# Performance work log

Measured on AMD Instinct MI355X. Metric: run time of the kernel, lower is better.

The kernel has to match this reference:

```python
import jax, jax.numpy as jnp
import numpy as np

B, L, D, H = 4, 512, 256, 128  # batch, seq_len, input_size, hidden_size
NEG = -1e30


def setup_inputs() -> dict:
    key = jax.random.key(0)
    ks = jax.random.split(key, 16)
    init = lambda k, shape, fan_in: (jax.random.normal(k, shape, jnp.float32) / np.sqrt(fan_in).astype(np.float32))
    v = jax.random.normal(ks[0], (B, L, D), jnp.float32)
    lengths = jax.random.randint(ks[1], (B,), L // 2, L + 1).astype(jnp.int32)
    p_mask = (jnp.arange(L)[None, :] < lengths[:, None])  # [B, L] bool
    return {
        "v": v,
        "lengths": lengths,
        "p_mask": p_mask,
        "own_W": init(ks[2], (H, D), D), "own_b": jnp.zeros((H,), jnp.float32),
        "comp_W": init(ks[3], (H, D), D), "comp_b": jnp.zeros((H,), jnp.float32),
        "v_attn": init(ks[4], (H,), H),
        "gate_W": init(ks[5], (2 * D, 2 * D), 2 * D), "gate_b": jnp.zeros((2 * D,), jnp.float32),
        "w_ih_f": init(ks[6], (3 * H, 2 * D), 2 * D), "w_hh_f": init(ks[7], (3 * H, H), H),
        "b_ih_f": jnp.zeros((3 * H,), jnp.float32), "b_hh_f": jnp.zeros((3 * H,), jnp.float32),
        "w_ih_b": init(ks[8], (3 * H, 2 * D), 2 * D), "w_hh_b": init(ks[9], (3 * H, H), H),
        "b_ih_b": jnp.zeros((3 * H,), jnp.float32), "b_hh_b": jnp.zeros((3 * H,), jnp.float32),
    }


def _gru(x, tmask, w_ih, w_hh, b_ih, b_hh, reverse):
    """Single-direction GRU over [B, L, In] with length masking (emulates packing)."""
    Bn, Ln, _ = x.shape
    Hn = w_hh.shape[1]
    xp = jnp.einsum('bli,hi->blh', x, w_ih) + b_ih  # [B, L, 3H] input projections

    def step(h, inputs):
        xpt, m = inputs  # [B, 3H], [B, 1]
        hp = h @ w_hh.T + b_hh
        xr, xz, xn = jnp.split(xpt, 3, axis=-1)
        hr, hz, hn = jnp.split(hp, 3, axis=-1)
        r = jax.nn.sigmoid(xr + hr)
        z = jax.nn.sigmoid(xz + hz)
        n = jnp.tanh(xn + r * hn)
        h_new = (1.0 - z) * n + z * h
        h = jnp.where(m, h_new, h)
        return h, jnp.where(m, h_new, jnp.zeros_like(h_new))

    h0 = jnp.zeros((Bn, Hn), x.dtype)
    xs = (jnp.swapaxes(xp, 0, 1), tmask.T[:, :, None])
    _, outs = jax.lax.scan(step, h0, xs, reverse=reverse)
    return jnp.swapaxes(outs, 0, 1)  # [B, L, H]


def reference(v, lengths, p_mask, own_W, own_b, comp_W, comp_b, v_attn,
              gate_W, gate_b, w_ih_f, w_hh_f, b_ih_f, b_hh_f,
              w_ih_b, w_hh_b, b_ih_b, b_hh_b):
    # Additive (Bahdanau / RNet) self-attention, vectorized over all query positions.
    own = v @ own_W.T + own_b    # [B, L, H] (query term)
    comp = v @ comp_W.T + comp_b  # [B, L, H] (key term)
    # scores[b, q, k] = tanh(own_q + comp_k) . v_attn
    scores = jnp.einsum('bqkh,h->bqk', jnp.tanh(own[:, :, None, :] + comp[:, None, :, :]), v_attn)
    scores = jnp.where(p_mask[:, None, :], scores, NEG)  # mask padded keys
    attn = jax.nn.softmax(scores, axis=2)
    C = jnp.einsum('bqk,bkd->bqd', attn, v)  # attended context
    inp = jnp.concatenate([v, C], axis=-1)   # [B, L, 2D]
    inp = jax.nn.sigmoid(inp @ gate_W.T + gate_b) * inp  # gating
    # Bidirectional GRU encoder (pack_padded emulated via time mask; eval mode, no dropout).
    tmask = (jnp.arange(inp.shape[1])[None, :] < lengths[:, None])
    out_f = _gru(inp, tmask, w_ih_f, w_hh_f, b_ih_f, b_hh_f, reverse=False)
    out_b = _gru(inp, tmask, w_ih_b, w_hh_b, b_ih_b, b_hh_b, reverse=True)
    return jnp.concatenate([out_f, out_b], axis=-1)  # [B, L, 2H]
```

## Files before the change

### kernel.cpp

```cpp
#include <hip/hip_runtime.h>
#include <hip/hip_bf16.h>

#define NEGINF -1e30f

typedef __attribute__((ext_vector_type(8))) short short8;
typedef __attribute__((ext_vector_type(4))) float f32x4;

__device__ __forceinline__ float fast_sigmoid(float x) {
    return __builtin_amdgcn_rcpf(1.f + __expf(-x));
}
__device__ __forceinline__ float fast_tanh(float x) {
    return 1.f - 2.f * __builtin_amdgcn_rcpf(1.f + __expf(2.f * x));
}
__device__ __forceinline__ short f2bf(float f) {
    unsigned u = __float_as_uint(f);
    return (short)((u + 0x7fff + ((u >> 16) & 1)) >> 16);
}
__device__ __forceinline__ float bf2f(short b) {
    return __uint_as_float(((unsigned)(unsigned short)b) << 16);
}

__device__ __forceinline__ void bar_lds() {
    asm volatile("s_waitcnt lgkmcnt(0)\n\ts_barrier" ::: "memory");
}

__global__ __launch_bounds__(256) void gemm_bias(
    const float* __restrict__ A,
    const float* __restrict__ W1, const float* __restrict__ b1, float* __restrict__ out1,
    const float* __restrict__ W2, const float* __restrict__ b2, float* __restrict__ out2,
    const int* __restrict__ lengths,
    int M, int N, int K, int nsplit, int mode) {
    const int m0 = blockIdx.y * 64;
    if ((m0 & 511) >= lengths[m0 >> 9]) return;
    __shared__ __align__(16) short Abh[2][2048];
    __shared__ __align__(16) short Abl[2][2048];
    __shared__ __align__(16) short Bbh[2][2048];
    __shared__ __align__(16) short Bbl[2][2048];
    const int tid = threadIdx.x;
    int bx = blockIdx.x;
    const float* W = W1; const float* bias = b1; float* out = out1;
    int n0;
    if (bx < nsplit) {
        n0 = bx * 64;
    } else {
        W = W2; bias = b2; out = out2;
        n0 = (bx - nsplit) * 64;
    }
    const int wave = tid >> 6;
    const int lane = tid & 63;
    const int mrow = lane & 15;
    const int quad = lane >> 4;
    const int wm = (wave >> 1) * 32;
    const int wn = (wave & 1) * 32;

    const int r_ = tid >> 2;
    const int sg = (tid & 3) * 8;

    f32x4 acc[2][2];
#pragma unroll
    for (int mt = 0; mt < 2; mt++)
#pragma unroll
        for (int nt = 0; nt < 2; nt++) acc[mt][nt] = (f32x4){0.f, 0.f, 0.f, 0.f};

    float4 a0 = *(const float4*)(A + (size_t)(m0 + r_) * K + sg);
    float4 a1 = *(const float4*)(A + (size_t)(m0 + r_) * K + sg + 4);
    float4 w0 = *(const float4*)(W + (size_t)(n0 + r_) * K + sg);
    float4 w1 = *(const float4*)(W + (size_t)(n0 + r_) * K + sg + 4);

    for (int k0 = 0; k0 < K; k0 += 32) {
        const int cur = (k0 >> 5) & 1;
        {
            float av[8] = {a0.x, a0.y, a0.z, a0.w, a1.x, a1.y, a1.z, a1.w};
            float wv[8] = {w0.x, w0.y, w0.z, w0.w, w1.x, w1.y, w1.z, w1.w};
            short8 ah, al, bh, bl;
#pragma unroll
            for (int j = 0; j < 8; j++) {
                short h = f2bf(av[j]); ah[j] = h; al[j] = f2bf(av[j] - bf2f(h));
                short g = f2bf(wv[j]); bh[j] = g; bl[j] = f2bf(wv[j] - bf2f(g));
            }
            *(short8*)&Abh[cur][r_ * 32 + sg] = ah;
            *(short8*)&Abl[cur][r_ * 32 + sg] = al;
            *(short8*)&Bbh[cur][r_ * 32 + sg] = bh;
            *(short8*)&Bbl[cur][r_ * 32 + sg] = bl;
        }
        if (k0 + 32 < K) {
            a0 = *(const float4*)(A + (size_t)(m0 + r_) * K + k0 + 32 + sg);
            a1 = *(const float4*)(A + (size_t)(m0 + r_) * K + k0 + 32 + sg + 4);
            w0 = *(const float4*)(W + (size_t)(n0 + r_) * K + k0 + 32 + sg);
            w1 = *(const float4*)(W + (size_t)(n0 + r_) * K + k0 + 32 + sg + 4);
        }
        bar_lds();
        short8 Ah[2], Al[2], Bh[2], Bl[2];
#pragma unroll
        for (int t = 0; t < 2; t++) {
            int ar = (wm + t * 16 + mrow) * 32 + quad * 8;
            int br = (wn + t * 16 + mrow) * 32 + quad * 8;
            Ah[t] = *(const short8*)&Abh[cur][ar];
            Al[t] = *(const short8*)&Abl[cur][ar];
            Bh[t] = *(const short8*)&Bbh[cur][br];
            Bl[t] = *(const short8*)&Bbl[cur][br];
        }
#pragma unroll
        for (int mt = 0; mt < 2; mt++)
#pragma unroll
            for (int nt = 0; nt < 2; nt++) {
                acc[mt][nt] = __builtin_amdgcn_mfma_f32_16x16x32_bf16(Ah[mt], Bh[nt], acc[mt][nt], 0, 0, 0);
                acc[mt][nt] = __builtin_amdgcn_mfma_f32_16x16x32_bf16(Al[mt], Bh[nt], acc[mt][nt], 0, 0, 0);
                acc[mt][nt] = __builtin_amdgcn_mfma_f32_16x16x32_bf16(Ah[mt], Bl[nt], acc[mt][nt], 0, 0, 0);
            }
        bar_lds();
    }
    float bsv[2];
#pragma unroll
    for (int nt = 0; nt < 2; nt++) bsv[nt] = bias[n0 + wn + nt * 16 + mrow];
#pragma unroll
    for (int mt = 0; mt < 2; mt++)
#pragma unroll
        for (int nt = 0; nt < 2; nt++) {
            int n = n0 + wn + nt * 16 + mrow;
#pragma unroll
            for (int r = 0; r < 4; r++) {
                int m = m0 + wm + mt * 16 + quad * 4 + r;
                float val = acc[mt][nt][r] + bsv[nt];
                if (mode == 1) val = fast_sigmoid(val) * A[(size_t)m * K + n];
                out[(size_t)m * N + n] = val;
            }
        }
}

__global__ __launch_bounds__(512) void attn_kernel(
    const float* __restrict__ v, const int* __restrict__ lengths,
    const float* __restrict__ own, const float* __restrict__ comp,
    const float* __restrict__ v_attn, float* __restrict__ inp) {
    const int L = 512, D = 256, H = 128;
    const int b = blockIdx.x >> 6;
    const int q0 = (blockIdx.x & 63) * 8;
    const int len = lengths[b];
    if (q0 >= len) return;
    const int tid = threadIdx.x;
    const float K2E = 2.8853900817779268f;
    __shared__ __align__(16) float oKT[128 * 8];
    __shared__ float va2s[128];
    __shared__ __align__(16) float scf[512 * 12];
    __shared__ float inv8[8];

    for (int i = tid; i < 1024; i += 512) {
        int qq = i >> 7, hh = i & 127;
        oKT[hh * 8 + qq] = K2E * own[((size_t)(b * L + q0 + qq)) * H + hh];
    }
    if (tid < 128) va2s[tid] = -2.f * v_attn[tid];
    __syncthreads();

    {
        const int k = tid;
        float acc[8];
#pragma unroll
        for (int q = 0; q < 8; q++) acc[q] = 0.f;
        if (k < len) {
            const float* cp = comp + ((size_t)(b * L + k)) * H;
            for (int h = 0; h < 128; h += 4) {
                float4 c4 = *(const float4*)(cp + h);
                const float* cv = (const float*)&c4;
#pragma unroll
                for (int j = 0; j < 4; j++) {
                    float cK = cv[j] * K2E;
                    float va = va2s[h + j];
                    float4 o0 = *(const float4*)&oKT[(h + j) * 8];
                    float4 o1 = *(const float4*)&oKT[(h + j) * 8 + 4];
                    const float* op0 = (const float*)&o0;
                    const float* op1 = (const float*)&o1;
#pragma unroll
                    for (int q = 0; q < 4; q++) {
                        float r = __builtin_amdgcn_rcpf(1.f + exp2f(cK + op0[q]));
                        acc[q] = fmaf(va, r, acc[q]);
                    }
#pragma unroll
                    for (int q = 0; q < 4; q++) {
                        float r = __builtin_amdgcn_rcpf(1.f + exp2f(cK + op1[q]));
                        acc[4 + q] = fmaf(va, r, acc[4 + q]);
                    }
                }
            }
#pragma unroll
            for (int q = 0; q < 8; q++) acc[q] = __expf(acc[q]);
        }
        *(float4*)&scf[k * 12] = *(float4*)&acc[0];
        *(float4*)&scf[k * 12 + 4] = *(float4*)&acc[4];
    }
    __syncthreads();

    {
        int w = tid >> 6, l = tid & 63;
        float s = 0.f;
#pragma unroll
        for (int kk = 0; kk < 8; kk++) s += scf[(l + kk * 64) * 12 + w];
#pragma unroll
        for (int off = 1; off < 64; off <<= 1) s += __shfl_xor(s, off);
        if (l == 0) inv8[w] = __builtin_amdgcn_rcpf(s);
    }
    __syncthreads();

    {
        const int d = tid & 255;
        const int qh = tid >> 8;
        float c0 = 0.f, c1 = 0.f, c2 = 0.f, c3 = 0.f;
        const float* vb = v + ((size_t)b * L) * D + d;
        for (int k = 0; k < L; k += 2) {
            float v0 = vb[(size_t)k * D];
            float v1 = vb[(size_t)(k + 1) * D];
            float4 s0 = *(const float4*)&scf[k * 12 + qh * 4];
            float4 s1 = *(const float4*)&scf[(k + 1) * 12 + qh * 4];
            c0 += s0.x * v0 + s1.x * v1;
            c1 += s0.y * v0 + s1.y * v1;
            c2 += s0.z * v0 + s1.z * v1;
            c3 += s0.w * v0 + s1.w * v1;
        }
        float cc[4] = {c0, c1, c2, c3};
#pragma unroll
        for (int j = 0; j < 4; j++) {
            int q = q0 + qh * 4 + j;
            size_t row = ((size_t)(b * L + q)) * 512;
            inp[row + 256 + d] = cc[j] * inv8[qh * 4 + j];
            inp[row + d] = v[((size_t)(b * L + q)) * D + d];
        }
    }
}

__global__ __launch_bounds__(512, 2) void gru_kernel(
    const float* __restrict__ xp_f, const float* __restrict__ xp_b,
    const float* __restrict__ w_hh_f, const float* __restrict__ w_hh_b,
    const float* __restrict__ b_hh_f, const float* __restrict__ b_hh_b,
    const int* __restrict__ lengths, float* __restrict__ out) {
    const int L = 512, H = 128;
    const int dir = blockIdx.x >> 2;
    const int b = blockIdx.x & 3;
    const float* xp = dir ? xp_b : xp_f;
    const float* w_hh = dir ? w_hh_b : w_hh_f;
    const float* b_hh = dir ? b_hh_b : b_hh_f;
    const int tid = threadIdx.x;
    const int wave = tid >> 6;
    const int lane = tid & 63;
    const int mrow = lane & 15;
    const int quad = lane >> 4;
    const int jj = 16 * wave + lane;

    __shared__ __align__(16) short hbuf[2][256];
    __shared__ __align__(16) float xbuf[16 * 384];
    __shared__ __align__(16) float obuf[16 * 128];

    short8 wb[3][4];
#pragma unroll
    for (int g = 0; g < 3; g++) {
        int row = g * 128 + 16 * wave + mrow;
#pragma unroll
        for (int kt = 0; kt < 4; kt++) {
            const float* wp = w_hh + (size_t)row * H + kt * 32 + quad * 8;
            float4 w0 = *(const float4*)(wp);
            float4 w1 = *(const float4*)(wp + 4);
            float wv[8] = {w0.x, w0.y, w0.z, w0.w, w1.x, w1.y, w1.z, w1.w};
            short8 hi8;
#pragma unroll
            for (int k = 0; k < 8; k++) hi8[k] = f2bf(wv[k]);
            wb[g][kt] = hi8;
        }
    }
    float br = 0.f, bz = 0.f, bn = 0.f, hcur = 0.f;
    if (lane < 16) {
        br = b_hh[jj];
        bz = b_hh[128 + jj];
        bn = b_hh[256 + jj];
    }

    const int len = lengths[b];
    for (int idx = tid; idx < (L - len) * 128; idx += 512) {
        int tt = len + (idx >> 7);
        int kk = idx & 127;
        out[((size_t)(b * L + tt)) * 256 + dir * 128 + kk] = 0.f;
    }
    if (tid < 256) hbuf[0][tid] = 0;

    const int f1 = tid + 512, f2 = tid + 1024;
    const int sA = tid / 96, jA = (tid % 96) * 4;
    const int sB = f1 / 96, jB = (f1 % 96) * 4;
    const int sC = f2 / 96, jC = (f2 % 96) * 4;

    const int nch = (len + 15) >> 4;
    float4 r0, r1, r2;
    {
        int tA = dir ? (len - 1 - sA) : sA;
        int tB = dir ? (len - 1 - sB) : sB;
        int tC = dir ? (len - 1 - sC) : sC;
        r0 = *(const float4*)&xp[((size_t)(b * L + tA)) * 384 + jA];
        r1 = *(const float4*)&xp[((size_t)(b * L + tB)) * 384 + jB];
        r2 = *(const float4*)&xp[((size_t)(b * L + tC)) * 384 + jC];
    }
    __syncthreads();

    const int bbase = (mrow & 1) * 128 + quad * 8;
    int par = 0;

    for (int c = 0; c < nch; c++) {
        const int cnt = min(16, len - c * 16);
        if (sA < cnt) *(float4*)&xbuf[sA * 384 + jA] = r0;
        if (sB < cnt) *(float4*)&xbuf[sB * 384 + jB] = r1;
        if (sC < cnt) *(float4*)&xbuf[sC * 384 + jC] = r2;
        if (c > 0) {
            int p0 = (c - 1) * 16;
            for (int i = tid; i < 16 * 128; i += 512) {
                int ss = i >> 7, kk = i & 127;
                int tt = dir ? (len - 1 - (p0 + ss)) : (p0 + ss);
                out[((size_t)(b * L + tt)) * 256 + dir * 128 + kk] = obuf[i];
            }
        }
        if (c + 1 < nch) {
            int ncnt = min(16, len - (c + 1) * 16);
            int base = (c + 1) * 16;
            if (sA < ncnt) {
                int tt = dir ? (len - 1 - (base + sA)) : (base + sA);
                r0 = *(const float4*)&xp[((size_t)(b * L + tt)) * 384 + jA];
            }
            if (sB < ncnt) {
                int tt = dir ? (len - 1 - (base + sB)) : (base + sB);
                r1 = *(const float4*)&xp[((size_t)(b * L + tt)) * 384 + jB];
            }
            if (sC < ncnt) {
                int tt = dir ? (len - 1 - (base + sC)) : (base + sC);
                r2 = *(const float4*)&xp[((size_t)(b * L + tt)) * 384 + jC];
            }
        }
        bar_lds();
        for (int s = 0; s < cnt; s++) {
            float xr, xz, xn;
            if (lane < 16) {
                xr = xbuf[s * 384 + jj];
                xz = xbuf[s * 384 + 128 + jj];
                xn = xbuf[s * 384 + 256 + jj];
            }
            short8 af[4];
#pragma unroll
            for (int kt = 0; kt < 4; kt++) af[kt] = *(const short8*)&hbuf[par][bbase + kt * 32];
            f32x4 acc[3];
#pragma unroll
            for (int g = 0; g < 3; g++) acc[g] = (f32x4){0.f, 0.f, 0.f, 0.f};
#pragma unroll
            for (int kt = 0; kt < 4; kt++)
#pragma unroll
                for (int g = 0; g < 3; g++)
                    acc[g] = __builtin_amdgcn_mfma_f32_16x16x32_bf16(af[kt], wb[g][kt], acc[g], 0, 0, 0);
            if (lane < 16) {
                float hr = acc[0][0] + acc[0][1] + br;
                float hz = acc[1][0] + acc[1][1] + bz;
                float hh = acc[2][0] + acc[2][1] + bn;
                float r = fast_sigmoid(xr + hr);
                float z = fast_sigmoid(xz + hz);
                float n = fast_tanh(xn + r * hh);
                float hn = (1.f - z) * n + z * hcur;
                hcur = hn;
                short hb = f2bf(hn);
                hbuf[par ^ 1][jj] = hb;
                hbuf[par ^ 1][128 + jj] = f2bf(hn - bf2f(hb));
                obuf[s * 128 + jj] = hn;
            }
            par ^= 1;
            bar_lds();
        }
    }
    {
        int p0 = (nch - 1) * 16;
        int pcnt = len - p0;
        for (int i = tid; i < pcnt * 128; i += 512) {
            int ss = i >> 7, kk = i & 127;
            int tt = dir ? (len - 1 - (p0 + ss)) : (p0 + ss);
            out[((size_t)(b * L + tt)) * 256 + dir * 128 + kk] = obuf[i];
        }
    }
}

extern "C" void kernel_launch(void* const* d_in, const int* in_sizes, int n_in,
                              void* d_out, int out_size, void* d_ws, size_t ws_size,
                              hipStream_t stream) {
    const int B = 4, L = 512, D = 256, H = 128;
    const int M = B * L;

    const float* v      = (const float*)d_in[0];
    const int* lengths  = (const int*)d_in[1];
    const float* own_W  = (const float*)d_in[3];
    const float* own_b  = (const float*)d_in[4];
    const float* comp_W = (const float*)d_in[5];
    const float* comp_b = (const float*)d_in[6];
    const float* v_attn = (const float*)d_in[7];
    const float* gate_W = (const float*)d_in[8];
    const float* gate_b = (const float*)d_in[9];
    const float* w_ih_f = (const float*)d_in[10];
    const float* w_hh_f = (const float*)d_in[11];
    const float* b_ih_f = (const float*)d_in[12];
    const float* b_hh_f = (const float*)d_in[13];
    const float* w_ih_b = (const float*)d_in[14];
    const float* w_hh_b = (const float*)d_in[15];
    const float* b_ih_b = (const float*)d_in[16];
    const float* b_hh_b = (const float*)d_in[17];

    float* ws   = (float*)d_ws;
    float* own  = ws;
    float* comp = own + (size_t)M * H;
    float* inp  = comp + (size_t)M * H;
    float* gated = inp + (size_t)M * 512;
    float* xp_f = gated + (size_t)M * 512;
    float* xp_b = xp_f + (size_t)M * 384;
    float* out  = (float*)d_out;

    gemm_bias<<<dim3(4, M / 64), 256, 0, stream>>>(
        v, own_W, own_b, own, comp_W, comp_b, comp, lengths, M, H, D, 2, 0);
    attn_kernel<<<dim3(B * 64), 512, 0, stream>>>(v, lengths, own, comp, v_attn, inp);
    gemm_bias<<<dim3(8, M / 64), 256, 0, stream>>>(
        inp, gate_W, gate_b, gated, gate_W, gate_b, gated, lengths, M, 512, 512, 8, 1);
    gemm_bias<<<dim3(12, M / 64), 256, 0, stream>>>(
        gated, w_ih_f, b_ih_f, xp_f, w_ih_b, b_ih_b, xp_b, lengths, M, 384, 512, 6, 0);
    gru_kernel<<<dim3(8), 512, 0, stream>>>(xp_f, xp_b, w_hh_f, w_hh_b, b_hh_f, b_hh_b, lengths, out);
}
```

Measured before the change: 399.6 us.

## Fuse all stages into one cooperative persistent kernel with grid syncs

Replaces the five separate launches with a single cooperative kernel of 256 blocks of 512 threads. It runs the projection GEMMs, attention, gating GEMM, input-projection GEMM and the GRU recurrence as phases separated by grid.sync, with a shared-memory union across phases. The GEMM tile is reworked for 8 waves, each computing a 32x16 sub-tile with 4-wide loads, and the trailing barrier of each K-step is dropped. The goal is to remove per-launch overhead and inter-kernel gaps. In exchange it pays grid-wide barrier costs, forces occupancy to one block per CU, and leaves most blocks idle during the long GRU phase.

```diff
diff --git a/kernel.cpp b/kernel.cpp
--- a/kernel.cpp
+++ b/kernel.cpp
@@ -1,9 +1,11 @@
 #include <hip/hip_runtime.h>
 #include <hip/hip_bf16.h>
-
-#define NEGINF -1e30f
+#include <hip/hip_cooperative_groups.h>
+
+namespace cg = cooperative_groups;
 
 typedef __attribute__((ext_vector_type(8))) short short8;
+typedef __attribute__((ext_vector_type(4))) short short4_t;
 typedef __attribute__((ext_vector_type(4))) float f32x4;
 
 __device__ __forceinline__ float fast_sigmoid(float x) {
@@ -19,136 +21,107 @@
 __device__ __forceinline__ float bf2f(short b) {
     return __uint_as_float(((unsigned)(unsigned short)b) << 16);
 }
-
 __device__ __forceinline__ void bar_lds() {
     asm volatile("s_waitcnt lgkmcnt(0)\n\ts_barrier" ::: "memory");
 }
 
-__global__ __launch_bounds__(256) void gemm_bias(
-    const float* __restrict__ A,
-    const float* __restrict__ W1, const float* __restrict__ b1, float* __restrict__ out1,
-    const float* __restrict__ W2, const float* __restrict__ b2, float* __restrict__ out2,
-    const int* __restrict__ lengths,
-    int M, int N, int K, int nsplit, int mode) {
-    const int m0 = blockIdx.y * 64;
-    if ((m0 & 511) >= lengths[m0 >> 9]) return;
-    __shared__ __align__(16) short Abh[2][2048];
-    __shared__ __align__(16) short Abl[2][2048];
-    __shared__ __align__(16) short Bbh[2][2048];
-    __shared__ __align__(16) short Bbl[2][2048];
+struct __align__(16) GemmSh { short Abh[2][2048]; short Abl[2][2048];
+                              short Bbh[2][2048]; short Bbl[2][2048]; };
+struct __align__(16) AttnSh { float oKT[1024]; float va2s[128]; float inv8[8];
+                              float scf[6144]; };
+struct __align__(16) GruSh  { short hbuf[2][256]; float xbuf[6144];
+                              float obuf[2048]; };
+union __align__(16) SharedMem { GemmSh g; AttnSh a; GruSh r; };
+
+__device__ void gemm_tile(GemmSh& sh,
+                          const float* __restrict__ A, const float* __restrict__ W,
+                          const float* __restrict__ bias, float* __restrict__ out,
+                          int m0, int n0, int N, int K, int mode) {
     const int tid = threadIdx.x;
-    int bx = blockIdx.x;
-    const float* W = W1; const float* bias = b1; float* out = out1;
-    int n0;
-    if (bx < nsplit) {
-        n0 = bx * 64;
-    } else {
-        W = W2; bias = b2; out = out2;
-        n0 = (bx - nsplit) * 64;
-    }
-    const int wave = tid >> 6;
-    const int lane = tid & 63;
-    const int mrow = lane & 15;
-    const int quad = lane >> 4;
-    const int wm = (wave >> 1) * 32;
-    const int wn = (wave & 1) * 32;
-
-    const int r_ = tid >> 2;
-    const int sg = (tid & 3) * 8;
-
-    f32x4 acc[2][2];
-#pragma unroll
-    for (int mt = 0; mt < 2; mt++)
-#pragma unroll
-        for (int nt = 0; nt < 2; nt++) acc[mt][nt] = (f32x4){0.f, 0.f, 0.f, 0.f};
-
-    float4 a0 = *(const float4*)(A + (size_t)(m0 + r_) * K + sg);
-    float4 a1 = *(const float4*)(A + (size_t)(m0 + r_) * K + sg + 4);
-    float4 w0 = *(const float4*)(W + (size_t)(n0 + r_) * K + sg);
-    float4 w1 = *(const float4*)(W + (size_t)(n0 + r_) * K + sg + 4);
+    const int wave = tid >> 6, lane = tid & 63;
+    const int mrow = lane & 15, quad = lane >> 4;
+    const int wm = (wave >> 2) * 32, wn = (wave & 3) * 16;
+    const int r_ = tid >> 3;
+    const int sg = (tid & 7) * 4;
+
+    bar_lds();
+
+    f32x4 acc[2];
+    acc[0] = (f32x4){0.f, 0.f, 0.f, 0.f};
+    acc[1] = (f32x4){0.f, 0.f, 0.f, 0.f};
+
+    float4 a = *(const float4*)(A + (size_t)(m0 + r_) * K + sg);
+    float4 w = *(const float4*)(W + (size_t)(n0 + r_) * K + sg);
 
     for (int k0 = 0; k0 < K; k0 += 32) {
         const int cur = (k0 >> 5) & 1;
         {
-            float av[8] = {a0.x, a0.y, a0.z, a0.w, a1.x, a1.y, a1.z, a1.w};
-            float wv[8] = {w0.x, w0.y, w0.z, w0.w, w1.x, w1.y, w1.z, w1.w};
-            short8 ah, al, bh, bl;
-#pragma unroll
-            for (int j = 0; j < 8; j++) {
+            float av[4] = {a.x, a.y, a.z, a.w};
+            float wv[4] = {w.x, w.y, w.z, w.w};
+            short4_t ah, al, bh, bl;
+#pragma unroll
+            for (int j = 0; j < 4; j++) {
                 short h = f2bf(av[j]); ah[j] = h; al[j] = f2bf(av[j] - bf2f(h));
                 short g = f2bf(wv[j]); bh[j] = g; bl[j] = f2bf(wv[j] - bf2f(g));
             }
-            *(short8*)&Abh[cur][r_ * 32 + sg] = ah;
-            *(short8*)&Abl[cur][r_ * 32 + sg] = al;
-            *(short8*)&Bbh[cur][r_ * 32 + sg] = bh;
-            *(short8*)&Bbl[cur][r_ * 32 + sg] = bl;
+            *(short4_t*)&sh.Abh[cur][r_ * 32 + sg] = ah;
+            *(short4_t*)&sh.Abl[cur][r_ * 32 + sg] = al;
+            *(short4_t*)&sh.Bbh[cur][r_ * 32 + sg] = bh;
+            *(short4_t*)&sh.Bbl[cur][r_ * 32 + sg] = bl;
         }
         if (k0 + 32 < K) {
-            a0 = *(const float4*)(A + (size_t)(m0 + r_) * K + k0 + 32 + sg);
-            a1 = *(const float4*)(A + (size_t)(m0 + r_) * K + k0 + 32 + sg + 4);
-            w0 = *(const float4*)(W + (size_t)(n0 + r_) * K + k0 + 32 + sg);
-            w1 = *(const float4*)(W + (size_t)(n0 + r_) * K + k0 + 32 + sg + 4);
+            a = *(const float4*)(A + (size_t)(m0 + r_) * K + k0 + 32 + sg);
+            w = *(const float4*)(W + (size_t)(n0 + r_) * K + k0 + 32 + sg);
         }
         bar_lds();
-        short8 Ah[2], Al[2], Bh[2], Bl[2];
-#pragma unroll
-        for (int t = 0; t < 2; t++) {
-            int ar = (wm + t * 16 + mrow) * 32 + quad * 8;
-            int br = (wn + t * 16 + mrow) * 32 + quad * 8;
-            Ah[t] = *(const short8*)&Abh[cur][ar];
-            Al[t] = *(const short8*)&Abl[cur][ar];
-            Bh[t] = *(const short8*)&Bbh[cur][br];
-            Bl[t] = *(const short8*)&Bbl[cur][br];
-        }
-#pragma unroll
-        for (int mt = 0; mt < 2; mt++)
-#pragma unroll
-            for (int nt = 0; nt < 2; nt++) {
-                acc[mt][nt] = __builtin_amdgcn_mfma_f32_16x16x32_bf16(Ah[mt], Bh[nt], acc[mt][nt], 0, 0, 0);
-                acc[mt][nt] = __builtin_amdgcn_mfma_f32_16x16x32_bf16(Al[mt], Bh[nt], acc[mt][nt], 0, 0, 0);
-                acc[mt][nt] = __builtin_amdgcn_mfma_f32_16x16x32_bf16(Ah[mt], Bl[nt], acc[mt][nt], 0, 0, 0);
-            }
-        bar_lds();
-    }
-    float bsv[2];
-#pragma unroll
-    for (int nt = 0; nt < 2; nt++) bsv[nt] = bias[n0 + wn + nt * 16 + mrow];
+        short8 Ah[2], Al[2];
+#pragma unroll
+        for (int mt = 0; mt < 2; mt++) {
+            int ar = (wm + mt * 16 + mrow) * 32 + quad * 8;
+            Ah[mt] = *(const short8*)&sh.Abh[cur][ar];
+            Al[mt] = *(const short8*)&sh.Abl[cur][ar];
+        }
+        int br = (wn + mrow) * 32 + quad * 8;
+        short8 Bh = *(const short8*)&sh.Bbh[cur][br];
+        short8 Bl = *(const short8*)&sh.Bbl[cur][br];
+#pragma unroll
+        for (int mt = 0; mt < 2; mt++) {
+            acc[mt] = __builtin_amdgcn_mfma_f32_16x16x32_bf16(Ah[mt], Bh, acc[mt], 0, 0, 0);
+            acc[mt] = __builtin_amdgcn_mfma_f32_16x16x32_bf16(Al[mt], Bh, acc[mt], 0, 0, 0);
+            acc[mt] = __builtin_amdgcn_mfma_f32_16x16x32_bf16(Ah[mt], Bl, acc[mt], 0, 0, 0);
+        }
+    }
+    const int n = n0 + wn + mrow;
+    const float bsv = bias[n];
 #pragma unroll
     for (int mt = 0; mt < 2; mt++)
 #pragma unroll
-        for (int nt = 0; nt < 2; nt++) {
-            int n = n0 + wn + nt * 16 + mrow;
-#pragma unroll
-            for (int r = 0; r < 4; r++) {
-                int m = m0 + wm + mt * 16 + quad * 4 + r;
-                float val = acc[mt][nt][r] + bsv[nt];
-                if (mode == 1) val = fast_sigmoid(val) * A[(size_t)m * K + n];
-                out[(size_t)m * N + n] = val;
-            }
-        }
-}
-
-__global__ __launch_bounds__(512) void attn_kernel(
-    const float* __restrict__ v, const int* __restrict__ lengths,
-    const float* __restrict__ own, const float* __restrict__ comp,
-    const float* __restrict__ v_attn, float* __restrict__ inp) {
+        for (int r = 0; r < 4; r++) {
+            int m = m0 + wm + mt * 16 + quad * 4 + r;
+            float val = acc[mt][r] + bsv;
+            if (mode == 1) val = fast_sigmoid(val) * A[(size_t)m * K + n];
+            out[(size_t)m * N + n] = val;
+        }
+}
+
+__device__ void attn_block(AttnSh& sh, const float* __restrict__ v,
+                           const int* __restrict__ lengths,
+                           const float* __restrict__ own, const float* __restrict__ comp,
+                           const float* __restrict__ v_attn, float* __restrict__ inp,
+                           int job) {
     const int L = 512, D = 256, H = 128;
-    const int b = blockIdx.x >> 6;
-    const int q0 = (blockIdx.x & 63) * 8;
+    const int b = job >> 6;
+    const int q0 = (job & 63) * 8;
     const int len = lengths[b];
     if (q0 >= len) return;
     const int tid = threadIdx.x;
     const float K2E = 2.8853900817779268f;
-    __shared__ __align__(16) float oKT[128 * 8];
-    __shared__ float va2s[128];
-    __shared__ __align__(16) float scf[512 * 12];
-    __shared__ float inv8[8];
 
     for (int i = tid; i < 1024; i += 512) {
         int qq = i >> 7, hh = i & 127;
-        oKT[hh * 8 + qq] = K2E * own[((size_t)(b * L + q0 + qq)) * H + hh];
-    }
-    if (tid < 128) va2s[tid] = -2.f * v_attn[tid];
+        sh.oKT[hh * 8 + qq] = K2E * own[((size_t)(b * L + q0 + qq)) * H + hh];
+    }
+    if (tid < 128) sh.va2s[tid] = -2.f * v_attn[tid];
     __syncthreads();
 
     {
@@ -164,9 +137,9 @@
 #pragma unroll
                 for (int j = 0; j < 4; j++) {
                     float cK = cv[j] * K2E;
-                    float va = va2s[h + j];
-                    float4 o0 = *(const float4*)&oKT[(h + j) * 8];
-                    float4 o1 = *(const float4*)&oKT[(h + j) * 8 + 4];
+                    float va = sh.va2s[h + j];
+                    float4 o0 = *(const float4*)&sh.oKT[(h + j) * 8];
+                    float4 o1 = *(const float4*)&sh.oKT[(h + j) * 8 + 4];
                     const float* op0 = (const float*)&o0;
                     const float* op1 = (const float*)&o1;
 #pragma unroll
@@ -184,8 +157,8 @@
 #pragma unroll
             for (int q = 0; q < 8; q++) acc[q] = __expf(acc[q]);
         }
-        *(float4*)&scf[k * 12] = *(float4*)&acc[0];
-        *(float4*)&scf[k * 12 + 4] = *(float4*)&acc[4];
+        *(float4*)&sh.scf[k * 12] = *(float4*)&acc[0];
+        *(float4*)&sh.scf[k * 12 + 4] = *(float4*)&acc[4];
     }
     __syncthreads();
 
@@ -193,10 +166,10 @@
         int w = tid >> 6, l = tid & 63;
         float s = 0.f;
 #pragma unroll
-        for (int kk = 0; kk < 8; kk++) s += scf[(l + kk * 64) * 12 + w];
+        for (int kk = 0; kk < 8; kk++) s += sh.scf[(l + kk * 64) * 12 + w];
 #pragma unroll
         for (int off = 1; off < 64; off <<= 1) s += __shfl_xor(s, off);
-        if (l == 0) inv8[w] = __builtin_amdgcn_rcpf(s);
+        if (l == 0) sh.inv8[w] = __builtin_amdgcn_rcpf(s);
     }
     __syncthreads();
 
@@ -208,8 +181,8 @@
         for (int k = 0; k < L; k += 2) {
             float v0 = vb[(size_t)k * D];
             float v1 = vb[(size_t)(k + 1) * D];
-            float4 s0 = *(const float4*)&scf[k * 12 + qh * 4];
-            float4 s1 = *(const float4*)&scf[(k + 1) * 12 + qh * 4];
+            float4 s0 = *(const float4*)&sh.scf[k * 12 + qh * 4];
+            float4 s1 = *(const float4*)&sh.scf[(k + 1) * 12 + qh * 4];
             c0 += s0.x * v0 + s1.x * v1;
             c1 += s0.y * v0 + s1.y * v1;
             c2 += s0.z * v0 + s1.z * v1;
@@ -220,20 +193,20 @@
         for (int j = 0; j < 4; j++) {
             int q = q0 + qh * 4 + j;
             size_t row = ((size_t)(b * L + q)) * 512;
-            inp[row + 256 + d] = cc[j] * inv8[qh * 4 + j];
+            inp[row + 256 + d] = cc[j] * sh.inv8[qh * 4 + j];
             inp[row + d] = v[((size_t)(b * L + q)) * D + d];
         }
     }
 }
 
-__global__ __launch_bounds__(512, 2) void gru_kernel(
-    const float* __restrict__ xp_f, const float* __restrict__ xp_b,
-    const float* __restrict__ w_hh_f, const float* __restrict__ w_hh_b,
-    const float* __restrict__ b_hh_f, const float* __restrict__ b_hh_b,
-    const int* __restrict__ lengths, float* __restrict__ out) {
+__device__ void gru_seq(GruSh& sh,
+                        const float* __restrict__ xp_f, const float* __restrict__ xp_b,
+                        const float* __restrict__ w_hh_f, const float* __restrict__ w_hh_b,
+                        const float* __restrict__ b_hh_f, const float* __restrict__ b_hh_b,
+                        const int* __restrict__ lengths, float* __restrict__ out, int idx) {
     const int L = 512, H = 128;
-    const int dir = blockIdx.x >> 2;
-    const int b = blockIdx.x & 3;
+    const int dir = idx >> 2;
+    const int b = idx & 3;
     const float* xp = dir ? xp_b : xp_f;
     const float* w_hh = dir ? w_hh_b : w_hh_f;
     const float* b_hh = dir ? b_hh_b : b_hh_f;
@@ -244,10 +217,6 @@
     const int quad = lane >> 4;
     const int jj = 16 * wave + lane;
 
-    __shared__ __align__(16) short hbuf[2][256];
-    __shared__ __align__(16) float xbuf[16 * 384];
-    __shared__ __align__(16) float obuf[16 * 128];
-
     short8 wb[3][4];
 #pragma unroll
     for (int g = 0; g < 3; g++) {
@@ -272,12 +241,12 @@
     }
 
     const int len = lengths[b];
-    for (int idx = tid; idx < (L - len) * 128; idx += 512) {
-        int tt = len + (idx >> 7);
-        int kk = idx & 127;
+    for (int i = tid; i < (L - len) * 128; i += 512) {
+        int tt = len + (i >> 7);
+        int kk = i & 127;
         out[((size_t)(b * L + tt)) * 256 + dir * 128 + kk] = 0.f;
     }
-    if (tid < 256) hbuf[0][tid] = 0;
+    if (tid < 256) sh.hbuf[0][tid] = 0;
 
     const int f1 = tid + 512, f2 = tid + 1024;
     const int sA = tid / 96, jA = (tid % 96) * 4;
@@ -301,15 +270,15 @@
 
     for (int c = 0; c < nch; c++) {
         const int cnt = min(16, len - c * 16);
-        if (sA < cnt) *(float4*)&xbuf[sA * 384 + jA] = r0;
-        if (sB < cnt) *(float4*)&xbuf[sB * 384 + jB] = r1;
-        if (sC < cnt) *(float4*)&xbuf[sC * 384 + jC] = r2;
+        if (sA < cnt) *(float4*)&sh.xbuf[sA * 384 + jA] = r0;
+        if (sB < cnt) *(float4*)&sh.xbuf[sB * 384 + jB] = r1;
+        if (sC < cnt) *(float4*)&sh.xbuf[sC * 384 + jC] = r2;
         if (c > 0) {
             int p0 = (c - 1) * 16;
             for (int i = tid; i < 16 * 128; i += 512) {
                 int ss = i >> 7, kk = i & 127;
                 int tt = dir ? (len - 1 - (p0 + ss)) : (p0 + ss);
-                out[((size_t)(b * L + tt)) * 256 + dir * 128 + kk] = obuf[i];
+                out[((size_t)(b * L + tt)) * 256 + dir * 128 + kk] = sh.obuf[i];
             }
         }
         if (c + 1 < nch) {
@@ -332,13 +301,13 @@
         for (int s = 0; s < cnt; s++) {
             float xr, xz, xn;
             if (lane < 16) {
-                xr = xbuf[s * 384 + jj];
-                xz = xbuf[s * 384 + 128 + jj];
-                xn = xbuf[s * 384 + 256 + jj];
+                xr = sh.xbuf[s * 384 + jj];
+                xz = sh.xbuf[s * 384 + 128 + jj];
+                xn = sh.xbuf[s * 384 + 256 + jj];
             }
             short8 af[4];
 #pragma unroll
-            for (int kt = 0; kt < 4; kt++) af[kt] = *(const short8*)&hbuf[par][bbase + kt * 32];
+            for (int kt = 0; kt < 4; kt++) af[kt] = *(const short8*)&sh.hbuf[par][bbase + kt * 32];
             f32x4 acc[3];
 #pragma unroll
             for (int g = 0; g < 3; g++) acc[g] = (f32x4){0.f, 0.f, 0.f, 0.f};
@@ -357,9 +326,9 @@
                 float hn = (1.f - z) * n + z * hcur;
                 hcur = hn;
                 short hb = f2bf(hn);
-                hbuf[par ^ 1][jj] = hb;
-                hbuf[par ^ 1][128 + jj] = f2bf(hn - bf2f(hb));
-                obuf[s * 128 + jj] = hn;
+                sh.hbuf[par ^ 1][jj] = hb;
+                sh.hbuf[par ^ 1][128 + jj] = f2bf(hn - bf2f(hb));
+                sh.obuf[s * 128 + jj] = hn;
             }
             par ^= 1;
             bar_lds();
@@ -371,16 +340,61 @@
         for (int i = tid; i < pcnt * 128; i += 512) {
             int ss = i >> 7, kk = i & 127;
             int tt = dir ? (len - 1 - (p0 + ss)) : (p0 + ss);
-            out[((size_t)(b * L + tt)) * 256 + dir * 128 + kk] = obuf[i];
-        }
-    }
+            out[((size_t)(b * L + tt)) * 256 + dir * 128 + kk] = sh.obuf[i];
+        }
+    }
+}
+
+__global__ __launch_bounds__(512, 1) void mega_kernel(
+    const float* v, const int* lengths,
+    const float* own_W, const float* own_b,
+    const float* comp_W, const float* comp_b,
+    const float* v_attn,
+    const float* gate_W, const float* gate_b,
+    const float* w_ih_f, const float* b_ih_f,
+    const float* w_hh_f, const float* b_hh_f,
+    const float* w_ih_b, const float* b_ih_b,
+    const float* w_hh_b, const float* b_hh_b,
+    float* own, float* comp, float* inp, float* gated,
+    float* xp_f, float* xp_b, float* out) {
+    __shared__ SharedMem sh;
+    cg::grid_group grid = cg::this_grid();
+    const int blk = blockIdx.x;
+
+    if (blk < 128) {
+        int bx = blk & 3, by = blk >> 2;
+        int m0 = by * 64;
+        if ((m0 & 511) < lengths[m0 >> 9]) {
+            if (bx < 2) gemm_tile(sh.g, v, own_W, own_b, own, m0, bx * 64, 128, 256, 0);
+            else        gemm_tile(sh.g, v, comp_W, comp_b, comp, m0, (bx - 2) * 64, 128, 256, 0);
+        }
+    }
+    grid.sync();
+    attn_block(sh.a, v, lengths, own, comp, v_attn, inp, blk);
+    grid.sync();
+    {
+        int bx = blk & 7, by = blk >> 3;
+        int m0 = by * 64;
+        if ((m0 & 511) < lengths[m0 >> 9])
+            gemm_tile(sh.g, inp, gate_W, gate_b, gated, m0, bx * 64, 512, 512, 1);
+    }
+    grid.sync();
+    for (int j = blk; j < 384; j += 256) {
+        int bx = j % 12, by = j / 12;
+        int m0 = by * 64;
+        if ((m0 & 511) >= lengths[m0 >> 9]) continue;
+        if (bx < 6) gemm_tile(sh.g, gated, w_ih_f, b_ih_f, xp_f, m0, bx * 64, 384, 512, 0);
+        else        gemm_tile(sh.g, gated, w_ih_b, b_ih_b, xp_b, m0, (bx - 6) * 64, 384, 512, 0);
+    }
+    grid.sync();
+    if (blk < 8)
+        gru_seq(sh.r, xp_f, xp_b, w_hh_f, w_hh_b, b_hh_f, b_hh_b, lengths, out, blk);
 }
 
 extern "C" void kernel_launch(void* const* d_in, const int* in_sizes, int n_in,
                               void* d_out, int out_size, void* d_ws, size_t ws_size,
                               hipStream_t stream) {
-    const int B = 4, L = 512, D = 256, H = 128;
-    const int M = B * L;
+    const int M = 2048, H = 128;
 
     const float* v      = (const float*)d_in[0];
     const int* lengths  = (const int*)d_in[1];
@@ -400,21 +414,25 @@
     const float* b_ih_b = (const float*)d_in[16];
     const float* b_hh_b = (const float*)d_in[17];
 
-    float* ws   = (float*)d_ws;
-    float* own  = ws;
-    float* comp = own + (size_t)M * H;
-    float* inp  = comp + (size_t)M * H;
+    float* ws    = (float*)d_ws;
+    float* own   = ws;
+    float* comp  = own + (size_t)M * H;
+    float* inp   = comp + (size_t)M * H;
     float* gated = inp + (size_t)M * 512;
-    float* xp_f = gated + (size_t)M * 512;
-    float* xp_b = xp_f + (size_t)M * 384;
-    float* out  = (float*)d_out;
-
-    gemm_bias<<<dim3(4, M / 64), 256, 0, stream>>>(
-        v, own_W, own_b, own, comp_W, comp_b, comp, lengths, M, H, D, 2, 0);
-    attn_kernel<<<dim3(B * 64), 512, 0, stream>>>(v, lengths, own, comp, v_attn, inp);
-    gemm_bias<<<dim3(8, M / 64), 256, 0, stream>>>(
-        inp, gate_W, gate_b, gated, gate_W, gate_b, gated, lengths, M, 512, 512, 8, 1);
-    gemm_bias<<<dim3(12, M / 64), 256, 0, stream>>>(
-        gated, w_ih_f, b_ih_f, xp_f, w_ih_b, b_ih_b, xp_b, lengths, M, 384, 512, 6, 0);
-    gru_kernel<<<dim3(8), 512, 0, stream>>>(xp_f, xp_b, w_hh_f, w_hh_b, b_hh_f, b_hh_b, lengths, out);
-}
+    float* xp_f  = gated + (size_t)M * 512;
+    float* xp_b  = xp_f + (size_t)M * 384;
+    float* outp  = (float*)d_out;
+
+    void* kargs[] = {
+        (void*)&v, (void*)&lengths,
+        (void*)&own_W, (void*)&own_b, (void*)&comp_W, (void*)&comp_b,
+        (void*)&v_attn, (void*)&gate_W, (void*)&gate_b,
+        (void*)&w_ih_f, (void*)&b_ih_f, (void*)&w_hh_f, (void*)&b_hh_f,
+        (void*)&w_ih_b, (void*)&b_ih_b, (void*)&w_hh_b, (void*)&b_hh_b,
+        (void*)&own, (void*)&comp, (void*)&inp, (void*)&gated,
+        (void*)&xp_f, (void*)&xp_b, (void*)&outp
+    };
+    hipError_t err = hipLaunchCooperativeKernel((void*)mega_kernel, dim3(256), dim3(512),
+                                                kargs, 0, stream);
+    (void)err;
+}
```

New measurement: 540.0 us. +35.1%, slower.

## Keep GRU input projections in registers and write outputs directly per step

Applied to the files above, without the earlier changes.

The GRU recurrence kernel no longer stages input projections and outputs through shared memory. Each active lane now prefetches the next 16 timesteps of its gate inputs into registers and writes each hidden state straight to global memory. The hidden-state buffer is padded to 320 entries so the hi/lo halves sit at offset 160, which is meant to reduce LDS bank conflicts. This removes the per-chunk cooperative copy and its barrier, at the cost of many more registers (launch bounds lowered to one block per SM) and uncoalesced scalar global stores on the serial critical path.

```diff
diff --git a/kernel.cpp b/kernel.cpp
--- a/kernel.cpp
+++ b/kernel.cpp
@@ -226,7 +226,7 @@
     }
 }
 
-__global__ __launch_bounds__(512, 2) void gru_kernel(
+__global__ __launch_bounds__(512, 1) void gru_kernel(
     const float* __restrict__ xp_f, const float* __restrict__ xp_b,
     const float* __restrict__ w_hh_f, const float* __restrict__ w_hh_b,
     const float* __restrict__ b_hh_f, const float* __restrict__ b_hh_b,
@@ -244,9 +244,7 @@
     const int quad = lane >> 4;
     const int jj = 16 * wave + lane;
 
-    __shared__ __align__(16) short hbuf[2][256];
-    __shared__ __align__(16) float xbuf[16 * 384];
-    __shared__ __align__(16) float obuf[16 * 128];
+    __shared__ __align__(16) short hbuf[2][320];
 
     short8 wb[3][4];
 #pragma unroll
@@ -272,106 +270,85 @@
     }
 
     const int len = lengths[b];
-    for (int idx = tid; idx < (L - len) * 128; idx += 512) {
-        int tt = len + (idx >> 7);
-        int kk = idx & 127;
+    for (int i = tid; i < (L - len) * 128; i += 512) {
+        int tt = len + (i >> 7);
+        int kk = i & 127;
         out[((size_t)(b * L + tt)) * 256 + dir * 128 + kk] = 0.f;
     }
-    if (tid < 256) hbuf[0][tid] = 0;
-
-    const int f1 = tid + 512, f2 = tid + 1024;
-    const int sA = tid / 96, jA = (tid % 96) * 4;
-    const int sB = f1 / 96, jB = (f1 % 96) * 4;
-    const int sC = f2 / 96, jC = (f2 % 96) * 4;
+    if (tid < 320) hbuf[0][tid] = 0;
 
     const int nch = (len + 15) >> 4;
-    float4 r0, r1, r2;
-    {
-        int tA = dir ? (len - 1 - sA) : sA;
-        int tB = dir ? (len - 1 - sB) : sB;
-        int tC = dir ? (len - 1 - sC) : sC;
-        r0 = *(const float4*)&xp[((size_t)(b * L + tA)) * 384 + jA];
-        r1 = *(const float4*)&xp[((size_t)(b * L + tB)) * 384 + jB];
-        r2 = *(const float4*)&xp[((size_t)(b * L + tC)) * 384 + jC];
+    float xr[16], xz[16], xn[16];
+    if (lane < 16) {
+#pragma unroll
+        for (int s = 0; s < 16; s++) {
+            if (s < len) {
+                int t = dir ? (len - 1 - s) : s;
+                size_t base = ((size_t)(b * L + t)) * 384;
+                xr[s] = xp[base + jj];
+                xz[s] = xp[base + 128 + jj];
+                xn[s] = xp[base + 256 + jj];
+            }
+        }
     }
     __syncthreads();
 
-    const int bbase = (mrow & 1) * 128 + quad * 8;
+    const int bbase = ((mrow & 1) ? 160 : 0) + quad * 8;
     int par = 0;
 
     for (int c = 0; c < nch; c++) {
         const int cnt = min(16, len - c * 16);
-        if (sA < cnt) *(float4*)&xbuf[sA * 384 + jA] = r0;
-        if (sB < cnt) *(float4*)&xbuf[sB * 384 + jB] = r1;
-        if (sC < cnt) *(float4*)&xbuf[sC * 384 + jC] = r2;
-        if (c > 0) {
-            int p0 = (c - 1) * 16;
-            for (int i = tid; i < 16 * 128; i += 512) {
-                int ss = i >> 7, kk = i & 127;
-                int tt = dir ? (len - 1 - (p0 + ss)) : (p0 + ss);
-                out[((size_t)(b * L + tt)) * 256 + dir * 128 + kk] = obuf[i];
-            }
-        }
-        if (c + 1 < nch) {
-            int ncnt = min(16, len - (c + 1) * 16);
-            int base = (c + 1) * 16;
-            if (sA < ncnt) {
-                int tt = dir ? (len - 1 - (base + sA)) : (base + sA);
-                r0 = *(const float4*)&xp[((size_t)(b * L + tt)) * 384 + jA];
-            }
-            if (sB < ncnt) {
-                int tt = dir ? (len - 1 - (base + sB)) : (base + sB);
-                r1 = *(const float4*)&xp[((size_t)(b * L + tt)) * 384 + jB];
-            }
-            if (sC < ncnt) {
-                int tt = dir ? (len - 1 - (base + sC)) : (base + sC);
-                r2 = *(const float4*)&xp[((size_t)(b * L + tt)) * 384 + jC];
-            }
-        }
-        bar_lds();
-        for (int s = 0; s < cnt; s++) {
-            float xr, xz, xn;
-            if (lane < 16) {
-                xr = xbuf[s * 384 + jj];
-                xz = xbuf[s * 384 + 128 + jj];
-                xn = xbuf[s * 384 + 256 + jj];
-            }
-            short8 af[4];
-#pragma unroll
-            for (int kt = 0; kt < 4; kt++) af[kt] = *(const short8*)&hbuf[par][bbase + kt * 32];
-            f32x4 acc[3];
-#pragma unroll
-            for (int g = 0; g < 3; g++) acc[g] = (f32x4){0.f, 0.f, 0.f, 0.f};
-#pragma unroll
-            for (int kt = 0; kt < 4; kt++)
-#pragma unroll
-                for (int g = 0; g < 3; g++)
-                    acc[g] = __builtin_amdgcn_mfma_f32_16x16x32_bf16(af[kt], wb[g][kt], acc[g], 0, 0, 0);
-            if (lane < 16) {
-                float hr = acc[0][0] + acc[0][1] + br;
-                float hz = acc[1][0] + acc[1][1] + bz;
-                float hh = acc[2][0] + acc[2][1] + bn;
-                float r = fast_sigmoid(xr + hr);
-                float z = fast_sigmoid(xz + hz);
-                float n = fast_tanh(xn + r * hh);
-                float hn = (1.f - z) * n + z * hcur;
-                hcur = hn;
-                short hb = f2bf(hn);
-                hbuf[par ^ 1][jj] = hb;
-                hbuf[par ^ 1][128 + jj] = f2bf(hn - bf2f(hb));
-                obuf[s * 128 + jj] = hn;
-            }
-            par ^= 1;
-            bar_lds();
-        }
-    }
-    {
-        int p0 = (nch - 1) * 16;
-        int pcnt = len - p0;
-        for (int i = tid; i < pcnt * 128; i += 512) {
-            int ss = i >> 7, kk = i & 127;
-            int tt = dir ? (len - 1 - (p0 + ss)) : (p0 + ss);
-            out[((size_t)(b * L + tt)) * 256 + dir * 128 + kk] = obuf[i];
+        float nxr[16], nxz[16], nxn[16];
+        if (lane < 16 && c + 1 < nch) {
+#pragma unroll
+            for (int s = 0; s < 16; s++) {
+                int rr = (c + 1) * 16 + s;
+                if (rr < len) {
+                    int t = dir ? (len - 1 - rr) : rr;
+                    size_t base = ((size_t)(b * L + t)) * 384;
+                    nxr[s] = xp[base + jj];
+                    nxz[s] = xp[base + 128 + jj];
+                    nxn[s] = xp[base + 256 + jj];
+                }
+            }
+        }
+#pragma unroll
+        for (int s = 0; s < 16; s++) {
+            if (s < cnt) {
+                short8 af[4];
+#pragma unroll
+                for (int kt = 0; kt < 4; kt++)
+                    af[kt] = *(const short8*)&hbuf[par][bbase + kt * 32];
+                f32x4 acc[3];
+#pragma unroll
+                for (int g = 0; g < 3; g++) acc[g] = (f32x4){0.f, 0.f, 0.f, 0.f};
+#pragma unroll
+                for (int kt = 0; kt < 4; kt++)
+#pragma unroll
+                    for (int g = 0; g < 3; g++)
+                        acc[g] = __builtin_amdgcn_mfma_f32_16x16x32_bf16(af[kt], wb[g][kt], acc[g], 0, 0, 0);
+                if (lane < 16) {
+                    float hr = acc[0][0] + acc[0][1] + br;
+                    float hz = acc[1][0] + acc[1][1] + bz;
+                    float hh = acc[2][0] + acc[2][1] + bn;
+                    float r = fast_sigmoid(xr[s] + hr);
+                    float z = fast_sigmoid(xz[s] + hz);
+                    float n = fast_tanh(xn[s] + r * hh);
+                    float hn = (1.f - z) * n + z * hcur;
+                    hcur = hn;
+                    short hb = f2bf(hn);
+                    hbuf[par ^ 1][jj] = hb;
+                    hbuf[par ^ 1][160 + jj] = f2bf(hn - bf2f(hb));
+                    int t = dir ? (len - 1 - (c * 16 + s)) : (c * 16 + s);
+                    out[((size_t)(b * L + t)) * 256 + dir * 128 + jj] = hn;
+                }
+                par ^= 1;
+                bar_lds();
+            }
+        }
+        if (lane < 16 && c + 1 < nch) {
+#pragma unroll
+            for (int s = 0; s < 16; s++) { xr[s] = nxr[s]; xz[s] = nxz[s]; xn[s] = nxn[s]; }
         }
     }
 }
```

New measurement: 384.4 us. 1.04x faster.
